# Kernel tuning notes

Hardware: AMD Instinct MI355X
Metric: run time of the kernel (lower is better)

The kernel has to match this reference:

```python
import jax, jax.numpy as jnp
import numpy as np

ALL_PERMS = jnp.array([[0, 1, 2], [0, 2, 1], [1, 0, 2], [1, 2, 0], [2, 0, 1], [2, 1, 0]], dtype=jnp.int32)
ENRICH_CLIP = 100.0
B, D, H = 16384, 512, 512
P_IN = D + 6 + 3   # seq_embed + pres_state(6) + round_onehot(3)
F_IN = D + 12 + 3  # seq_embed + full_state(12) + round_onehot(3)


def _gelu(x):
    return jax.nn.gelu(x, approximate=False)  # keras 'gelu' is erf-based


def _mlp3(x, w1, b1, w2, b2, w3, b3):
    h = _gelu(x @ w1 + b1)
    h = _gelu(h @ w2 + b2)
    return h @ w3 + b3


def setup_inputs() -> dict:
    key = jax.random.key(0)
    ks = jax.random.split(key, 12)
    s = 0.02
    return {
        'seq_embed': jax.random.normal(ks[0], (B, D), jnp.float32),
        'freq': jax.random.normal(ks[1], (B, 3), jnp.float32),
        'pres': (jax.random.uniform(ks[2], (B, 3)) < 0.5).astype(jnp.float32),
        'enrich': jax.random.normal(ks[3], (B, 3), jnp.float32),
        'pw1': jax.random.normal(ks[4], (P_IN, H), jnp.float32) * s, 'pb1': jnp.zeros((H,), jnp.float32),
        'pw2': jax.random.normal(ks[5], (H, H // 2), jnp.float32) * s, 'pb2': jnp.zeros((H // 2,), jnp.float32),
        'pw3': jax.random.normal(ks[6], (H // 2, 1), jnp.float32) * s, 'pb3': jnp.zeros((1,), jnp.float32),
        'fw1': jax.random.normal(ks[7], (F_IN, H), jnp.float32) * s, 'fb1': jnp.zeros((H,), jnp.float32),
        'fw2': jax.random.normal(ks[8], (H, H), jnp.float32) * s, 'fb2': jnp.zeros((H,), jnp.float32),
        'fw3': jax.random.normal(ks[9], (H, 2), jnp.float32) * s, 'fb3': jnp.zeros((2,), jnp.float32),
        'perm_idx': jax.random.randint(ks[10], (B,), 0, 6, dtype=jnp.int32),
        'round_mask': jax.random.randint(ks[11], (B, 3), 0, 2, dtype=jnp.int32),
    }


def _decode(seq_embed, freq, pres, enrich, mask_f, perms,
            pw1, pb1, pw2, pb2, pw3, pb3, fw1, fb1, fw2, fb2, fw3, fb3):
    Bn = seq_embed.shape[0]
    dt = seq_embed.dtype
    ones = jnp.ones((Bn,), dt)
    pres_state = jnp.zeros((Bn, 3, 2), dt)  # [R, (pres, decoded_flag)]
    full_state = jnp.zeros((Bn, 3, 4), dt)  # [R, (freq, pres, enrich, decoded_flag)]
    d_f = jnp.zeros((Bn, 3), dt)
    d_p = jnp.zeros((Bn, 3), dt)
    d_e = jnp.zeros((Bn, 3), dt)
    lf = lp = le = nm = jnp.float32(0.0)
    for step in range(3):
        ridx = perms[:, step]                               # [B]
        r_oh = jax.nn.one_hot(ridx, 3, dtype=dt)            # [B,3]
        take = lambda a: jnp.take_along_axis(a, ridx[:, None], axis=1)[:, 0]
        gt_f, gt_p, gt_e, m = take(freq), take(pres), take(enrich), take(mask_f)
        pres_inp = jnp.concatenate([seq_embed, pres_state.reshape(Bn, 6), r_oh], axis=1)
        pp_logit = _mlp3(pres_inp, pw1, pb1, pw2, pb2, pw3, pb3)[:, 0]
        fe_inp = jnp.concatenate([seq_embed, full_state.reshape(Bn, 12), r_oh], axis=1)
        fe_pred = _mlp3(fe_inp, fw1, fb1, fw2, fb2, fw3, fb3)
        pf, pe = fe_pred[:, 0], fe_pred[:, 1]
        lf = lf + jnp.sum(jnp.square(pf - gt_f) * m)
        bce = jnp.maximum(pp_logit, 0.0) - pp_logit * gt_p + jnp.log1p(jnp.exp(-jnp.abs(pp_logit)))
        lp = lp + jnp.sum(bce * m)
        le = le + jnp.sum(jnp.square(pe - gt_e) * m)
        nm = nm + jnp.sum(m)
        msk = m > 0.5
        act_f = jnp.where(msk, jnp.clip(pf, -10.0, 10.0), gt_f)
        act_p = jnp.where(msk, jax.nn.sigmoid(pp_logit), gt_p)
        act_e = jnp.where(msk, jnp.clip(pe, -ENRICH_CLIP, ENRICH_CLIP), gt_e)
        sel = r_oh[:, :, None]  # equal-mask scatter into the ridx-th slot
        pres_state = pres_state * (1.0 - sel) + jnp.stack([act_p, ones], axis=1)[:, None, :] * sel
        full_state = full_state * (1.0 - sel) + jnp.stack([act_f, act_p, act_e, ones], axis=1)[:, None, :] * sel
        d_f = d_f * (1.0 - r_oh) + act_f[:, None] * r_oh
        d_p = d_p * (1.0 - r_oh) + act_p[:, None] * r_oh
        d_e = d_e * (1.0 - r_oh) + act_e[:, None] * r_oh
    nm = nm + 1e-08
    return lf / nm, lp / nm, le / nm, d_f, d_p, d_e


def reference(seq_embed, freq, pres, enrich,
              pw1, pb1, pw2, pb2, pw3, pb3,
              fw1, fb1, fw2, fb2, fw3, fb3,
              perm_idx, round_mask):
    perms = ALL_PERMS[perm_idx]                      # [B,3] random round orders
    mask_f = round_mask.astype(seq_embed.dtype)      # [B,3] 0/1 mask
    lf, lp, le, d_f, d_p, d_e = _decode(seq_embed, freq, pres, enrich, mask_f, perms,
                                        pw1, pb1, pw2, pb2, pw3, pb3,
                                        fw1, fb1, fw2, fb2, fw3, fb3)
    # flat layout: [loss_freq, loss_pres, loss_enrich, dec_freq(B*3), dec_pres(B*3), dec_enrich(B*3)]
    return jnp.concatenate([jnp.stack([lf, lp, le]), d_f.ravel(), d_p.ravel(), d_e.ravel()])
```

## Files before the change

kernel.cpp:

```cpp
#include <hip/hip_runtime.h>
#include <hip/hip_bf16.h>
#include <math.h>

#define BATCH 16384

typedef unsigned short u16;
typedef short bf16x8 __attribute__((ext_vector_type(8)));
typedef float f32x4 __attribute__((ext_vector_type(4)));
typedef u16 u16x8 __attribute__((ext_vector_type(8)));
typedef u16 u16x2 __attribute__((ext_vector_type(2)));

__constant__ int PERMS_C[6][3] = {{0,1,2},{0,2,1},{1,0,2},{1,2,0},{2,0,1},{2,1,0}};

__device__ inline float bf2f(u16 u) {
    unsigned int x = ((unsigned int)u) << 16;
    float f; __builtin_memcpy(&f, &x, 4); return f;
}
__device__ inline u16 f2bf(float f) {
    __hip_bfloat16 h = __float2bfloat16(f);
    u16 u; __builtin_memcpy(&u, &h, 2); return u;
}
__device__ inline float gelu_exact(float x) {
    return 0.5f * x * (1.0f + erff(x * 0.70710678118654752f));
}
__device__ __forceinline__ float gelu_fast(float x) {
    float t = x * (1.59576912f + x * x * 0.07135481f);
    return x / (1.0f + __expf(-t));
}

__device__ inline void gload_lds16(const u16* g, u16* l) {
    __builtin_amdgcn_global_load_lds(
        (const __attribute__((address_space(1))) unsigned int*)g,
        (__attribute__((address_space(3))) unsigned int*)l,
        16, 0, 0);
}

__global__ __launch_bounds__(256) void prep_kernel(
    const float* __restrict__ seq,
    const float* __restrict__ pw1, const float* __restrict__ pw2,
    const float* __restrict__ fw1, const float* __restrict__ fw2,
    const float* __restrict__ pb1, const float* __restrict__ pb2,
    const float* __restrict__ fb1, const float* __restrict__ fb2,
    u16* __restrict__ sb, u16* __restrict__ W1T, u16* __restrict__ W2T,
    float* __restrict__ bias1, float* __restrict__ bias2)
{
    const int N0 = BATCH * 512;
    const int N1 = 1024 * 512;
    const int N2 = 768 * 512;
    const int N3 = 1024;
    const int N4 = 768;
    int i = blockIdx.x * 256 + threadIdx.x;
    if (i < N0) { sb[i] = f2bf(seq[i]); return; }
    i -= N0;
    if (i < N1) {
        int n = i >> 9, k = i & 511;
        float v = (n < 512) ? pw1[(size_t)k * 512 + n] : fw1[(size_t)k * 512 + (n - 512)];
        W1T[i] = f2bf(v); return;
    }
    i -= N1;
    if (i < N2) {
        int n = i >> 9, k = i & 511;
        float v = (n < 256) ? pw2[(size_t)k * 256 + n] : fw2[(size_t)k * 512 + (n - 256)];
        W2T[i] = f2bf(v); return;
    }
    i -= N2;
    if (i < N3) { bias1[i] = (i < 512) ? pb1[i] : fb1[i - 512]; return; }
    i -= N3;
    if (i < N4) { bias2[i] = (i < 256) ? pb2[i] : fb2[i - 256]; return; }
}

__global__ __launch_bounds__(256) void gemm_bf16(
    const u16* __restrict__ A, int lda,
    const u16* __restrict__ Bt, const float* __restrict__ bias,
    u16* __restrict__ C, int M, int N, int K)
{
    __shared__ __align__(16) u16 As[128 * 64];
    __shared__ __align__(16) u16 Bs[128 * 64];

    const int bm = blockIdx.x * 128;
    const int bn = blockIdx.y * 128;

    const int tid = threadIdx.x;
    const int wv = tid >> 6;
    const int lane = tid & 63;
    const int wr = wv >> 1;
    const int wc = wv & 1;

    const int lrow = lane >> 3;
    const int lcol = (lane & 7) << 3;

    f32x4 acc[4][4];
#pragma unroll
    for (int i = 0; i < 4; ++i)
#pragma unroll
        for (int j = 0; j < 4; ++j) acc[i][j] = (f32x4){0.f, 0.f, 0.f, 0.f};

    for (int k0 = 0; k0 < K; k0 += 64) {
#pragma unroll
        for (int q = 0; q < 4; ++q) {
            const int c = wv * 4 + q;
            const int row = c * 8 + lrow;
            gload_lds16(&A[(size_t)(bm + row) * lda + k0 + lcol], &As[c * 512]);
            gload_lds16(&Bt[(size_t)(bn + row) * K + k0 + lcol], &Bs[c * 512]);
        }
        __syncthreads();

#pragma unroll
        for (int ks = 0; ks < 64; ks += 32) {
            int kk = ks + (lane >> 4) * 8;
            bf16x8 af[4], bfr[4];
#pragma unroll
            for (int i = 0; i < 4; ++i)
                af[i] = *reinterpret_cast<const bf16x8*>(&As[(wr * 64 + i * 16 + (lane & 15)) * 64 + kk]);
#pragma unroll
            for (int j = 0; j < 4; ++j)
                bfr[j] = *reinterpret_cast<const bf16x8*>(&Bs[(wc * 64 + j * 16 + (lane & 15)) * 64 + kk]);
#pragma unroll
            for (int i = 0; i < 4; ++i)
#pragma unroll
                for (int j = 0; j < 4; ++j)
                    acc[i][j] = __builtin_amdgcn_mfma_f32_16x16x32_bf16(af[i], bfr[j], acc[i][j], 0, 0, 0);
        }
        __syncthreads();
    }

    const int r4 = (lane >> 4) * 4;
    const int cn = lane & 15;
#pragma unroll
    for (int i = 0; i < 4; ++i) {
#pragma unroll
        for (int j = 0; j < 4; ++j) {
            int gcol = bn + wc * 64 + j * 16 + cn;
            float bsv = bias[gcol];
#pragma unroll
            for (int r = 0; r < 4; ++r) {
                int grow = bm + wr * 64 + i * 16 + r4 + r;
                C[(size_t)grow * N + gcol] = f2bf(acc[i][j][r] + bsv);
            }
        }
    }
}


template<int NS>
__device__ __forceinline__ void h1_phase(
    const float* __restrict__ wsrc, int cw0, int rh,
    const u16x2 (&zreg)[32], int gcol0, char* h1base,
    const float (*state)[20], const int* rid)
{
    float w[NS + 3][2];
#pragma unroll
    for (int r = 0; r < NS + 3; ++r) {
        float2 v = *reinterpret_cast<const float2*>(&wsrc[(size_t)r * 512 + cw0]);
        w[r][0] = v.x; w[r][1] = v.y;
    }
#pragma unroll
    for (int r = 0; r < 32; ++r) {
        const int row = rh * 32 + r;
        const int ridx = rid[row];
        float s[NS];
        if constexpr (NS == 6) {
            float4 a = *reinterpret_cast<const float4*>(&state[row][0]);
            float2 b = *reinterpret_cast<const float2*>(&state[row][4]);
            s[0] = a.x; s[1] = a.y; s[2] = a.z; s[3] = a.w; s[4] = b.x; s[5] = b.y;
        } else {
            float4 a = *reinterpret_cast<const float4*>(&state[row][8]);
            float4 b = *reinterpret_cast<const float4*>(&state[row][12]);
            float4 c = *reinterpret_cast<const float4*>(&state[row][16]);
            s[0] = a.x; s[1] = a.y; s[2]  = a.z; s[3]  = a.w;
            s[4] = b.x; s[5] = b.y; s[6]  = b.z; s[7]  = b.w;
            s[8] = c.x; s[9] = c.y; s[10] = c.z; s[11] = c.w;
        }
        float d0 = (ridx == 0) ? w[NS][0] : ((ridx == 1) ? w[NS + 1][0] : w[NS + 2][0]);
        float d1 = (ridx == 0) ? w[NS][1] : ((ridx == 1) ? w[NS + 1][1] : w[NS + 2][1]);
#pragma unroll
        for (int j = 0; j < NS; ++j) { d0 += s[j] * w[j][0]; d1 += s[j] * w[j][1]; }
        float h0 = gelu_fast(bf2f(zreg[r][0]) + d0);
        float h1 = gelu_fast(bf2f(zreg[r][1]) + d1);
        unsigned int packed = (unsigned int)f2bf(h0) | ((unsigned int)f2bf(h1) << 16);
        int byte = (row * 2048 + gcol0 * 2) ^ ((row & 7) << 4);
        *reinterpret_cast<unsigned int*>(h1base + byte) = packed;
    }
}

__global__ __launch_bounds__(1024, 4) void decode3(
    const u16* __restrict__ Z,
    const float* __restrict__ pw1s, const float* __restrict__ fw1s,
    const u16* __restrict__ W2T, const float* __restrict__ bias2,
    const float* __restrict__ pw3, const float* __restrict__ pb3,
    const float* __restrict__ fw3, const float* __restrict__ fb3,
    const float* __restrict__ freq, const float* __restrict__ presv,
    const float* __restrict__ enrich, const int* __restrict__ round_mask,
    const int* __restrict__ perm_idx,
    float* __restrict__ part, float* __restrict__ out)
{
    __shared__ __align__(16) u16 H1s[64 * 1024];
    __shared__ float redh[16][64][3];
    __shared__ __align__(16) float state_s[64][20];
    __shared__ int pidx_s[64];
    __shared__ int rid_s[64];

    const int tid = threadIdx.x;
    const int wv  = tid >> 6;
    const int l   = tid & 63;
    const int row0 = blockIdx.x * 64;

    const int ci   = tid & 511;
    const int rh   = tid >> 9;
    const int half = ci >> 8;
    const int cw0  = (ci & 255) * 2;
    const int gcol0 = ci * 2;
    char* h1base = reinterpret_cast<char*>(H1s);

    {
        float* ss = &state_s[0][0];
        for (int i = tid; i < 64 * 20; i += 1024) ss[i] = 0.f;
        if (tid < 64) {
            int pp = perm_idx[row0 + tid];
            pidx_s[tid] = pp;
            rid_s[tid] = PERMS_C[pp][0];
        }
    }

    u16x2 zreg[32];
#pragma unroll
    for (int r = 0; r < 32; ++r)
        zreg[r] = *reinterpret_cast<const u16x2*>(
            &Z[(size_t)(row0 + rh * 32 + r) * 1024 + gcol0]);

    __syncthreads();

    const int colbase = wv * 48;
    const bool needP = (colbase < 256);
    const bool needF = (colbase + 32) >= 256;

    float lf_acc = 0.f, bce_acc = 0.f, le_acc = 0.f, mm_acc = 0.f;

#pragma unroll 1
    for (int step = 0; step < 3; ++step) {
        if (half == 0)
            h1_phase<6>(pw1s, cw0, rh, zreg, gcol0, h1base, state_s, rid_s);
        else
            h1_phase<12>(fw1s, cw0, rh, zreg, gcol0, h1base, state_s, rid_s);
        __syncthreads();

        f32x4 acc[4][3];
#pragma unroll
        for (int rf = 0; rf < 4; ++rf)
#pragma unroll
            for (int cf = 0; cf < 3; ++cf) acc[rf][cf] = (f32x4){0.f, 0.f, 0.f, 0.f};

        const int ar = l & 15;
        const int ks = (l >> 4) * 8;
#pragma unroll 2
        for (int kf = 0; kf < 16; ++kf) {
            bf16x8 bfr[3];
#pragma unroll
            for (int cf = 0; cf < 3; ++cf) {
                int col = colbase + cf * 16 + ar;
                bfr[cf] = *reinterpret_cast<const bf16x8*>(&W2T[(size_t)col * 512 + kf * 32 + ks]);
            }
            bf16x8 afP[4], afF[4];
            if (needP) {
#pragma unroll
                for (int rf = 0; rf < 4; ++rf) {
                    int row = rf * 16 + ar;
                    int byte = (row * 2048 + (kf * 32 + ks) * 2) ^ ((row & 7) << 4);
                    afP[rf] = *reinterpret_cast<const bf16x8*>(h1base + byte);
                }
            }
            if (needF) {
#pragma unroll
                for (int rf = 0; rf < 4; ++rf) {
                    int row = rf * 16 + ar;
                    int byte = (row * 2048 + 1024 + (kf * 32 + ks) * 2) ^ ((row & 7) << 4);
                    afF[rf] = *reinterpret_cast<const bf16x8*>(h1base + byte);
                }
            }
#pragma unroll
            for (int cf = 0; cf < 3; ++cf) {
                const bool hf = (colbase + cf * 16) >= 256;
#pragma unroll
                for (int rf = 0; rf < 4; ++rf)
                    acc[rf][cf] = __builtin_amdgcn_mfma_f32_16x16x32_bf16(
                        hf ? afF[rf] : afP[rf], bfr[cf], acc[rf][cf], 0, 0, 0);
            }
        }

#pragma unroll
        for (int rf = 0; rf < 4; ++rf) {
            float hsp[4] = {0.f, 0.f, 0.f, 0.f};
            float hsf[4] = {0.f, 0.f, 0.f, 0.f};
            float hse[4] = {0.f, 0.f, 0.f, 0.f};
#pragma unroll
            for (int cf = 0; cf < 3; ++cf) {
                const int colc = colbase + cf * 16;
                const int col = colc + ar;
                const float b2 = bias2[col];
                if (colc < 256) {
                    const float w3 = pw3[col];
#pragma unroll
                    for (int g = 0; g < 4; ++g) {
                        float h = gelu_fast(acc[rf][cf][g] + b2);
                        hsp[g] += h * w3;
                    }
                } else {
                    const float wf = fw3[(col - 256) * 2];
                    const float we = fw3[(col - 256) * 2 + 1];
#pragma unroll
                    for (int g = 0; g < 4; ++g) {
                        float h = gelu_fast(acc[rf][cf][g] + b2);
                        hsf[g] += h * wf;
                        hse[g] += h * we;
                    }
                }
            }
#pragma unroll
            for (int g = 0; g < 4; ++g) {
                float a = hsp[g], b = hsf[g], c = hse[g];
#pragma unroll
                for (int m = 1; m < 16; m <<= 1) {
                    a += __shfl_xor(a, m);
                    b += __shfl_xor(b, m);
                    c += __shfl_xor(c, m);
                }
                if ((l & 15) == 0) {
                    int row = rf * 16 + (l >> 4) * 4 + g;
                    redh[wv][row][0] = a;
                    redh[wv][row][1] = b;
                    redh[wv][row][2] = c;
                }
            }
        }
        __syncthreads();

        if (wv == 0) {
            const int row = l;
            const int b = row0 + row;
            float sp = 0.f, sf = 0.f, se = 0.f;
#pragma unroll
            for (int w2 = 0; w2 < 16; ++w2) {
                sp += redh[w2][row][0];
                sf += redh[w2][row][1];
                se += redh[w2][row][2];
            }
            float logit = sp + pb3[0];
            float pf    = sf + fb3[0];
            float pe    = se + fb3[1];
            int ridx = rid_s[row];
            float gt_f = freq[b * 3 + ridx];
            float gt_p = presv[b * 3 + ridx];
            float gt_e = enrich[b * 3 + ridx];
            float m = (float)round_mask[b * 3 + ridx];
            lf_acc  += (pf - gt_f) * (pf - gt_f) * m;
            bce_acc += (fmaxf(logit, 0.f) - logit * gt_p + log1pf(expf(-fabsf(logit)))) * m;
            le_acc  += (pe - gt_e) * (pe - gt_e) * m;
            mm_acc  += m;
            bool msk = m > 0.5f;
            float act_f = msk ? fminf(fmaxf(pf, -10.f), 10.f) : gt_f;
            float act_p = msk ? 1.f / (1.f + expf(-logit)) : gt_p;
            float act_e = msk ? fminf(fmaxf(pe, -100.f), 100.f) : gt_e;
            state_s[row][ridx * 2 + 0] = act_p;
            state_s[row][ridx * 2 + 1] = 1.f;
            state_s[row][8 + ridx * 4 + 0] = act_f;
            state_s[row][8 + ridx * 4 + 1] = act_p;
            state_s[row][8 + ridx * 4 + 2] = act_e;
            state_s[row][8 + ridx * 4 + 3] = 1.f;
            out[3 + b * 3 + ridx] = act_f;
            out[3 + 3 * BATCH + b * 3 + ridx] = act_p;
            out[3 + 6 * BATCH + b * 3 + ridx] = act_e;
            if (step < 2) rid_s[row] = PERMS_C[pidx_s[row]][step + 1];
        }
        __syncthreads();
    }

    if (wv == 0) {
        for (int off = 32; off > 0; off >>= 1) {
            lf_acc  += __shfl_down(lf_acc, off);
            bce_acc += __shfl_down(bce_acc, off);
            le_acc  += __shfl_down(le_acc, off);
            mm_acc  += __shfl_down(mm_acc, off);
        }
        if (l == 0) {
            float4 v; v.x = lf_acc; v.y = bce_acc; v.z = le_acc; v.w = mm_acc;
            *reinterpret_cast<float4*>(&part[blockIdx.x * 4]) = v;
        }
    }
}

#define NPART (BATCH / 64)

__global__ __launch_bounds__(256) void finalize_kernel(
    const float* __restrict__ part, float* __restrict__ out)
{
    __shared__ float red[4][4];
    float a0 = 0.f, a1 = 0.f, a2 = 0.f, a3 = 0.f;
    for (int j = threadIdx.x; j < NPART; j += 256) {
        float4 v = *reinterpret_cast<const float4*>(&part[j * 4]);
        a0 += v.x; a1 += v.y; a2 += v.z; a3 += v.w;
    }
    for (int off = 32; off > 0; off >>= 1) {
        a0 += __shfl_down(a0, off);
        a1 += __shfl_down(a1, off);
        a2 += __shfl_down(a2, off);
        a3 += __shfl_down(a3, off);
    }
    const int wid = threadIdx.x >> 6, lane = threadIdx.x & 63;
    if (lane == 0) { red[wid][0] = a0; red[wid][1] = a1; red[wid][2] = a2; red[wid][3] = a3; }
    __syncthreads();
    if (threadIdx.x == 0) {
        float s0 = 0.f, s1 = 0.f, s2 = 0.f, s3 = 0.f;
#pragma unroll
        for (int w2 = 0; w2 < 4; ++w2) {
            s0 += red[w2][0]; s1 += red[w2][1]; s2 += red[w2][2]; s3 += red[w2][3];
        }
        float nm = s3 + 1e-8f;
        out[0] = s0 / nm;
        out[1] = s1 / nm;
        out[2] = s2 / nm;
    }
}

extern "C" void kernel_launch(void* const* d_in, const int* in_sizes, int n_in,
                              void* d_out, int out_size, void* d_ws, size_t ws_size,
                              hipStream_t stream)
{
    const float* seq       = (const float*)d_in[0];
    const float* freq      = (const float*)d_in[1];
    const float* presv     = (const float*)d_in[2];
    const float* enrich    = (const float*)d_in[3];
    const float* pw1       = (const float*)d_in[4];
    const float* pb1       = (const float*)d_in[5];
    const float* pw2       = (const float*)d_in[6];
    const float* pb2       = (const float*)d_in[7];
    const float* pw3       = (const float*)d_in[8];
    const float* pb3       = (const float*)d_in[9];
    const float* fw1       = (const float*)d_in[10];
    const float* fb1       = (const float*)d_in[11];
    const float* fw2       = (const float*)d_in[12];
    const float* fb2       = (const float*)d_in[13];
    const float* fw3       = (const float*)d_in[14];
    const float* fb3       = (const float*)d_in[15];
    const int*   perm_idx  = (const int*)d_in[16];
    const int*   round_mask= (const int*)d_in[17];
    float* out = (float*)d_out;

    char* w = (char*)d_ws;
    u16* sb  = (u16*)w;  w += (size_t)BATCH * 512 * 2;
    u16* Z   = (u16*)w;  w += (size_t)BATCH * 1024 * 2;
    u16* W1T = (u16*)w;  w += (size_t)1024 * 512 * 2;
    u16* W2T = (u16*)w;  w += (size_t)768 * 512 * 2;
    float* bias1 = (float*)w; w += 1024 * 4;
    float* bias2 = (float*)w; w += 768 * 4;
    float* part  = (float*)w;

    {
        const int total = BATCH * 512 + 1024 * 512 + 768 * 512 + 1024 + 768;
        int grid = (total + 255) / 256;
        prep_kernel<<<grid, 256, 0, stream>>>(seq, pw1, pw2, fw1, fw2, pb1, pb2, fb1, fb2,
                                              sb, W1T, W2T, bias1, bias2);
    }

    gemm_bf16<<<dim3(BATCH / 128, 1024 / 128), 256, 0, stream>>>(
        sb, 512, W1T, bias1, Z, BATCH, 1024, 512);

    decode3<<<NPART, 1024, 0, stream>>>(
        Z, pw1 + (size_t)512 * 512, fw1 + (size_t)512 * 512,
        W2T, bias2, pw3, pb3, fw3, fb3,
        freq, presv, enrich, round_mask, perm_idx, part, out);

    finalize_kernel<<<1, 256, 0, stream>>>(part, out);
}
```

Measured before the change: 437.0 us.

## Shrink decode3 blocks to 32 rows with 512 threads and wider per-wave column tiles

The decode kernel now handles 32 batch rows per block using 512 threads instead of 64 rows with 1024 threads. Each wave now covers 96 output columns over 2 row fragments, where before it covered 48 columns over 4 row fragments. The W2T fragment is loaded inside the column loop to keep register pressure down. Halving the LDS footprint and block size should allow more blocks per CU and finer scheduling. The cost is that each W2T fragment is reused over fewer rows, so global or L2 traffic for W2 per row doubles.

```diff
diff --git a/kernel.cpp b/kernel.cpp
--- a/kernel.cpp
+++ b/kernel.cpp
@@ -19,9 +19,6 @@
 __device__ inline u16 f2bf(float f) {
     __hip_bfloat16 h = __float2bfloat16(f);
     u16 u; __builtin_memcpy(&u, &h, 2); return u;
-}
-__device__ inline float gelu_exact(float x) {
-    return 0.5f * x * (1.0f + erff(x * 0.70710678118654752f));
 }
 __device__ __forceinline__ float gelu_fast(float x) {
     float t = x * (1.59576912f + x * x * 0.07135481f);
@@ -144,7 +141,7 @@
 
 template<int NS>
 __device__ __forceinline__ void h1_phase(
-    const float* __restrict__ wsrc, int cw0, int rh,
+    const float* __restrict__ wsrc, int cw0,
     const u16x2 (&zreg)[32], int gcol0, char* h1base,
     const float (*state)[20], const int* rid)
 {
@@ -155,8 +152,7 @@
         w[r][0] = v.x; w[r][1] = v.y;
     }
 #pragma unroll
-    for (int r = 0; r < 32; ++r) {
-        const int row = rh * 32 + r;
+    for (int row = 0; row < 32; ++row) {
         const int ridx = rid[row];
         float s[NS];
         if constexpr (NS == 6) {
@@ -175,15 +171,16 @@
         float d1 = (ridx == 0) ? w[NS][1] : ((ridx == 1) ? w[NS + 1][1] : w[NS + 2][1]);
 #pragma unroll
         for (int j = 0; j < NS; ++j) { d0 += s[j] * w[j][0]; d1 += s[j] * w[j][1]; }
-        float h0 = gelu_fast(bf2f(zreg[r][0]) + d0);
-        float h1 = gelu_fast(bf2f(zreg[r][1]) + d1);
+        float h0 = gelu_fast(bf2f(zreg[row][0]) + d0);
+        float h1 = gelu_fast(bf2f(zreg[row][1]) + d1);
         unsigned int packed = (unsigned int)f2bf(h0) | ((unsigned int)f2bf(h1) << 16);
         int byte = (row * 2048 + gcol0 * 2) ^ ((row & 7) << 4);
         *reinterpret_cast<unsigned int*>(h1base + byte) = packed;
     }
 }
 
-__global__ __launch_bounds__(1024, 4) void decode3(
+__global__ void __attribute__((amdgpu_flat_work_group_size(512, 512)))
+__attribute__((amdgpu_waves_per_eu(4, 4))) decode3(
     const u16* __restrict__ Z,
     const float* __restrict__ pw1s, const float* __restrict__ fw1s,
     const u16* __restrict__ W2T, const float* __restrict__ bias2,
@@ -194,28 +191,27 @@
     const int* __restrict__ perm_idx,
     float* __restrict__ part, float* __restrict__ out)
 {
-    __shared__ __align__(16) u16 H1s[64 * 1024];
-    __shared__ float redh[16][64][3];
-    __shared__ __align__(16) float state_s[64][20];
-    __shared__ int pidx_s[64];
-    __shared__ int rid_s[64];
+    __shared__ __align__(16) u16 H1s[32 * 1024];
+    __shared__ float redh[8][32][3];
+    __shared__ __align__(16) float state_s[32][20];
+    __shared__ int pidx_s[32];
+    __shared__ int rid_s[32];
 
     const int tid = threadIdx.x;
     const int wv  = tid >> 6;
     const int l   = tid & 63;
-    const int row0 = blockIdx.x * 64;
-
-    const int ci   = tid & 511;
-    const int rh   = tid >> 9;
-    const int half = ci >> 8;
-    const int cw0  = (ci & 255) * 2;
+    const int row0 = blockIdx.x * 32;
+
+    const int ci    = tid;
+    const int half  = ci >> 8;
+    const int cw0   = (ci & 255) * 2;
     const int gcol0 = ci * 2;
     char* h1base = reinterpret_cast<char*>(H1s);
 
     {
         float* ss = &state_s[0][0];
-        for (int i = tid; i < 64 * 20; i += 1024) ss[i] = 0.f;
-        if (tid < 64) {
+        for (int i = tid; i < 32 * 20; i += 512) ss[i] = 0.f;
+        if (tid < 32) {
             int pp = perm_idx[row0 + tid];
             pidx_s[tid] = pp;
             rid_s[tid] = PERMS_C[pp][0];
@@ -226,44 +222,38 @@
 #pragma unroll
     for (int r = 0; r < 32; ++r)
         zreg[r] = *reinterpret_cast<const u16x2*>(
-            &Z[(size_t)(row0 + rh * 32 + r) * 1024 + gcol0]);
+            &Z[(size_t)(row0 + r) * 1024 + gcol0]);
 
     __syncthreads();
 
-    const int colbase = wv * 48;
+    const int colbase = wv * 96;
     const bool needP = (colbase < 256);
-    const bool needF = (colbase + 32) >= 256;
+    const bool needF = (colbase + 80) >= 256;
 
     float lf_acc = 0.f, bce_acc = 0.f, le_acc = 0.f, mm_acc = 0.f;
 
 #pragma unroll 1
     for (int step = 0; step < 3; ++step) {
         if (half == 0)
-            h1_phase<6>(pw1s, cw0, rh, zreg, gcol0, h1base, state_s, rid_s);
+            h1_phase<6>(pw1s, cw0, zreg, gcol0, h1base, state_s, rid_s);
         else
-            h1_phase<12>(fw1s, cw0, rh, zreg, gcol0, h1base, state_s, rid_s);
+            h1_phase<12>(fw1s, cw0, zreg, gcol0, h1base, state_s, rid_s);
         __syncthreads();
 
-        f32x4 acc[4][3];
-#pragma unroll
-        for (int rf = 0; rf < 4; ++rf)
-#pragma unroll
-            for (int cf = 0; cf < 3; ++cf) acc[rf][cf] = (f32x4){0.f, 0.f, 0.f, 0.f};
+        f32x4 acc[2][6];
+#pragma unroll
+        for (int rf = 0; rf < 2; ++rf)
+#pragma unroll
+            for (int cf = 0; cf < 6; ++cf) acc[rf][cf] = (f32x4){0.f, 0.f, 0.f, 0.f};
 
         const int ar = l & 15;
         const int ks = (l >> 4) * 8;
 #pragma unroll 2
         for (int kf = 0; kf < 16; ++kf) {
-            bf16x8 bfr[3];
-#pragma unroll
-            for (int cf = 0; cf < 3; ++cf) {
-                int col = colbase + cf * 16 + ar;
-                bfr[cf] = *reinterpret_cast<const bf16x8*>(&W2T[(size_t)col * 512 + kf * 32 + ks]);
-            }
-            bf16x8 afP[4], afF[4];
+            bf16x8 afP[2], afF[2];
             if (needP) {
 #pragma unroll
-                for (int rf = 0; rf < 4; ++rf) {
+                for (int rf = 0; rf < 2; ++rf) {
                     int row = rf * 16 + ar;
                     int byte = (row * 2048 + (kf * 32 + ks) * 2) ^ ((row & 7) << 4);
                     afP[rf] = *reinterpret_cast<const bf16x8*>(h1base + byte);
@@ -271,29 +261,32 @@
             }
             if (needF) {
 #pragma unroll
-                for (int rf = 0; rf < 4; ++rf) {
+                for (int rf = 0; rf < 2; ++rf) {
                     int row = rf * 16 + ar;
                     int byte = (row * 2048 + 1024 + (kf * 32 + ks) * 2) ^ ((row & 7) << 4);
                     afF[rf] = *reinterpret_cast<const bf16x8*>(h1base + byte);
                 }
             }
 #pragma unroll
-            for (int cf = 0; cf < 3; ++cf) {
+            for (int cf = 0; cf < 6; ++cf) {
                 const bool hf = (colbase + cf * 16) >= 256;
-#pragma unroll
-                for (int rf = 0; rf < 4; ++rf)
+                int col = colbase + cf * 16 + ar;
+                bf16x8 bfr = *reinterpret_cast<const bf16x8*>(
+                    &W2T[(size_t)col * 512 + kf * 32 + ks]);
+#pragma unroll
+                for (int rf = 0; rf < 2; ++rf)
                     acc[rf][cf] = __builtin_amdgcn_mfma_f32_16x16x32_bf16(
-                        hf ? afF[rf] : afP[rf], bfr[cf], acc[rf][cf], 0, 0, 0);
-            }
-        }
-
-#pragma unroll
-        for (int rf = 0; rf < 4; ++rf) {
+                        hf ? afF[rf] : afP[rf], bfr, acc[rf][cf], 0, 0, 0);
+            }
+        }
+
+#pragma unroll
+        for (int rf = 0; rf < 2; ++rf) {
             float hsp[4] = {0.f, 0.f, 0.f, 0.f};
             float hsf[4] = {0.f, 0.f, 0.f, 0.f};
             float hse[4] = {0.f, 0.f, 0.f, 0.f};
 #pragma unroll
-            for (int cf = 0; cf < 3; ++cf) {
+            for (int cf = 0; cf < 6; ++cf) {
                 const int colc = colbase + cf * 16;
                 const int col = colc + ar;
                 const float b2 = bias2[col];
@@ -334,12 +327,12 @@
         }
         __syncthreads();
 
-        if (wv == 0) {
+        if (wv == 0 && l < 32) {
             const int row = l;
             const int b = row0 + row;
             float sp = 0.f, sf = 0.f, se = 0.f;
 #pragma unroll
-            for (int w2 = 0; w2 < 16; ++w2) {
+            for (int w2 = 0; w2 < 8; ++w2) {
                 sp += redh[w2][row][0];
                 sf += redh[w2][row][1];
                 se += redh[w2][row][2];
@@ -388,7 +381,7 @@
     }
 }
 
-#define NPART (BATCH / 64)
+#define NPART (BATCH / 32)
 
 __global__ __launch_bounds__(256) void finalize_kernel(
     const float* __restrict__ part, float* __restrict__ out)
@@ -464,7 +457,7 @@
     gemm_bf16<<<dim3(BATCH / 128, 1024 / 128), 256, 0, stream>>>(
         sb, 512, W1T, bias1, Z, BATCH, 1024, 512);
 
-    decode3<<<NPART, 1024, 0, stream>>>(
+    decode3<<<NPART, 512, 0, stream>>>(
         Z, pw1 + (size_t)512 * 512, fw1 + (size_t)512 * 512,
         W2T, bias2, pw3, pb3, fw3, fb3,
         freq, presv, enrich, round_mask, perm_idx, part, out);
```

Measured after the change: 455.7 us. +4.3%, slower.
